# Kernel tuning notes

Measured on AMD Instinct MI355X. Metric: run time of the kernel, lower is better.

Reference implementation:

```python
import jax, jax.numpy as jnp
import numpy as np

B = 2048
D = 40960          # util.half_kp_numel(): 64 king squares * 640 piece-square planes
BASE = 288
MOVE = 4096        # util.move_numel(): 64 from-squares * 64 to-squares
MOVE_SIZE = (64, 64)


def setup_inputs() -> dict:
    key = jax.random.key(0)
    ks = jax.random.split(key, 24)
    f32 = jnp.float32
    # forward args: sparse one-hot half-kp occupancy vectors (modeled as rand floats)
    pov = (jax.random.uniform(ks[0], (B, 1), f32) > 0.5).astype(f32)
    white = (jax.random.uniform(ks[1], (B, D), f32) < 0.001).astype(f32)
    black = (jax.random.uniform(ks[2], (B, D), f32) < 0.001).astype(f32)
    s = 0.01
    p = {
        'W_w': jax.random.normal(ks[3], (BASE, D), f32) * s,
        'b_w': jnp.zeros((BASE,), f32),
        'W_b': jax.random.normal(ks[4], (BASE, D), f32) * s,
        'b_b': jnp.zeros((BASE,), f32),
        'W_v0': jax.random.normal(ks[5], (32, 2 * BASE), f32) * s,
        'b_v0': jnp.zeros((32,), f32),
        'W_v1': jax.random.normal(ks[6], (32, 32), f32) * s,
        'b_v1': jnp.zeros((32,), f32),
        'W_v2': jax.random.normal(ks[7], (1, 32), f32) * s,
        'b_v2': jnp.zeros((1,), f32),
        'W_a0': jax.random.normal(ks[8], (144, 2 * BASE), f32) * s,
        'b_a0': jnp.zeros((144,), f32),
        'W_a1': jax.random.normal(ks[9], (MOVE, 144), f32) * s,
        'b_a1': jnp.zeros((MOVE,), f32),
        'W_vs': jax.random.normal(ks[10], (1, 2 * BASE), f32) * s,
        'b_vs': jnp.zeros((1,), f32),
        'W_as': jax.random.normal(ks[11], (MOVE, 2 * BASE), f32) * s,
        'b_as': jnp.zeros((MOVE,), f32),
    }
    return dict(pov=pov, white=white, black=black, **p)


def _linear(x, W, b):
    return x @ W.T + b


def reference(pov, white, black, W_w, b_w, W_b, b_b,
              W_v0, b_v0, W_v1, b_v1, W_v2, b_v2,
              W_a0, b_a0, W_a1, b_a1, W_vs, b_vs, W_as, b_as):
    # half-kp affine accumulators (the sparse gather-sum candidate)
    w256 = _linear(white, W_w, b_w)            # [B, BASE]
    b256 = _linear(black, W_b, b_b)            # [B, BASE]
    cat_wb = jnp.concatenate([w256, b256], axis=1)
    cat_bw = jnp.concatenate([b256, w256], axis=1)
    base = jax.nn.relu(pov * cat_wb + (1.0 - pov) * cat_bw)  # [B, 2*BASE]
    # value head with skip
    val = jax.nn.relu(_linear(base, W_v0, b_v0))
    val = jax.nn.relu(_linear(val, W_v1, b_v1))
    val = _linear(val, W_v2, b_v2) + _linear(base, W_vs, b_vs)   # [B, 1]
    # action head with skip
    act = jax.nn.relu(_linear(base, W_a0, b_a0))
    act = _linear(act, W_a1, b_a1) + _linear(base, W_as, b_as)   # [B, MOVE]
    act = act.reshape(act.shape[0], *MOVE_SIZE)                  # [B, 64, 64]
    return (val, act)
```

## Files before the change

### kernel.cpp

```cpp
#include <hip/hip_runtime.h>

#define D_IN 40960
#define NB 2048
#define BASEN 288
#define CAPL 95
#define KP 736

typedef __attribute__((ext_vector_type(4))) float f32x4;
typedef __attribute__((ext_vector_type(8))) short short8;

__device__ inline float bf2f(ushort u) {
    unsigned v = ((unsigned)u) << 16; float f; __builtin_memcpy(&f, &v, 4); return f;
}
__device__ inline ushort f2bf(float f) {
    unsigned x; __builtin_memcpy(&x, &f, 4);
    unsigned r = (x + 0x7FFFu + ((x >> 16) & 1u)) >> 16; return (ushort)r;
}

__device__ inline void llds16(const void* g, void* l) {
    __builtin_amdgcn_global_load_lds((const __attribute__((address_space(1))) unsigned*)g,
                                     (__attribute__((address_space(3))) unsigned*)l, 16, 0, 0);
}

__global__ __launch_bounds__(256) void transpose_kernel(const float* __restrict__ Ww,
                                                        const float* __restrict__ Wb,
                                                        ushort* __restrict__ Wtw,
                                                        ushort* __restrict__ Wtb) {
    const float* src = blockIdx.z ? Wb : Ww;
    ushort* dst = blockIdx.z ? Wtb : Wtw;
    __shared__ float tile[32][65];
    int i = threadIdx.x;
    int d0 = blockIdx.x * 64, o0 = blockIdx.y * 32;
    int tr = i >> 4, tc4 = (i & 15) * 4;
#pragma unroll
    for (int rep = 0; rep < 2; ++rep) {
        int row = tr + rep * 16;
        float4 u = *(const float4*)&src[(size_t)(o0 + row) * D_IN + d0 + tc4];
        tile[row][tc4] = u.x; tile[row][tc4 + 1] = u.y; tile[row][tc4 + 2] = u.z; tile[row][tc4 + 3] = u.w;
    }
    __syncthreads();
    int dr = i >> 3, oc4 = (i & 7) * 4;
#pragma unroll
    for (int rep = 0; rep < 2; ++rep) {
        int d = dr + rep * 32;
        ushort4 u;
        u.x = f2bf(tile[oc4][d]); u.y = f2bf(tile[oc4 + 1][d]);
        u.z = f2bf(tile[oc4 + 2][d]); u.w = f2bf(tile[oc4 + 3][d]);
        *(ushort4*)&dst[(size_t)(d0 + d) * BASEN + o0 + oc4] = u;
    }
}

__global__ __launch_bounds__(256) void prep_kernel(const float* __restrict__ W_a1,
                                                   const float* __restrict__ W_as,
                                                   const float* __restrict__ b_a1,
                                                   const float* __restrict__ b_as,
                                                   const float* __restrict__ W_a0,
                                                   const float* __restrict__ W_v0,
                                                   ushort* __restrict__ Wcat,
                                                   float* __restrict__ biasA,
                                                   ushort* __restrict__ Wa0h,
                                                   ushort* __restrict__ Wv0h) {
    int m = blockIdx.x, t = threadIdx.x;
    if (m < 4096) {
        ushort* dst = Wcat + (size_t)m * KP;
        if (t < 144) dst[t] = f2bf(W_a1[(size_t)m * 144 + t]);
        if (t >= 144 && t < 160) dst[t] = 0;
        for (int j = t; j < 576; j += 256) dst[160 + j] = f2bf(W_as[(size_t)m * 576 + j]);
        if (t == 200) biasA[m] = b_a1[m] + b_as[m];
    } else if (m < 4096 + 144) {
        int r = m - 4096;
        for (int j = t; j < 576; j += 256) Wa0h[(size_t)r * 576 + j] = f2bf(W_a0[(size_t)r * 576 + j]);
    } else {
        int r = m - (4096 + 144);
        for (int j = t; j < 576; j += 256) Wv0h[(size_t)r * 576 + j] = f2bf(W_v0[(size_t)r * 576 + j]);
    }
}

__global__ __launch_bounds__(576) void row_kernel(const float* __restrict__ white,
                                                  const float* __restrict__ black,
                                                  const ushort* __restrict__ Wtw,
                                                  const ushort* __restrict__ Wtb,
                                                  const float* __restrict__ pov,
                                                  const float* __restrict__ b_w,
                                                  const float* __restrict__ b_b,
                                                  const ushort* __restrict__ Wa0h,
                                                  const float* __restrict__ b_a0,
                                                  const ushort* __restrict__ Wv0h,
                                                  const float* __restrict__ b_v0,
                                                  const float* __restrict__ W_v1,
                                                  const float* __restrict__ b_v1,
                                                  const float* __restrict__ W_v2,
                                                  const float* __restrict__ b_v2,
                                                  const float* __restrict__ W_vs,
                                                  const float* __restrict__ b_vs,
                                                  ushort* __restrict__ hidden,
                                                  float* __restrict__ outv) {
    int b = blockIdx.x, t = threadIdx.x;
    __shared__ int cntW, cntB;
    __shared__ int idxW[CAPL], idxB[CAPL];
    __shared__ float accS[576];
    __shared__ float baseS[576];
    __shared__ float v0s[32];
    __shared__ float skipS;
    if (t == 0) cntW = 0;
    if (t == 1) cntB = 0;
    __syncthreads();

    const uint4* vw = (const uint4*)(white + (size_t)b * D_IN);
    const uint4* vb = (const uint4*)(black + (size_t)b * D_IN);
    for (int i = t; i < D_IN / 4; i += 576) {
        uint4 x = vw[i];
        if (x.x) { int p = atomicAdd(&cntW, 1); if (p < CAPL) idxW[p] = i * 4; }
        if (x.y) { int p = atomicAdd(&cntW, 1); if (p < CAPL) idxW[p] = i * 4 + 1; }
        if (x.z) { int p = atomicAdd(&cntW, 1); if (p < CAPL) idxW[p] = i * 4 + 2; }
        if (x.w) { int p = atomicAdd(&cntW, 1); if (p < CAPL) idxW[p] = i * 4 + 3; }
        uint4 y = vb[i];
        if (y.x) { int p = atomicAdd(&cntB, 1); if (p < CAPL) idxB[p] = i * 4; }
        if (y.y) { int p = atomicAdd(&cntB, 1); if (p < CAPL) idxB[p] = i * 4 + 1; }
        if (y.z) { int p = atomicAdd(&cntB, 1); if (p < CAPL) idxB[p] = i * 4 + 2; }
        if (y.w) { int p = atomicAdd(&cntB, 1); if (p < CAPL) idxB[p] = i * 4 + 3; }
    }
    __syncthreads();

    {
        int col = (t < 288) ? t : t - 288;
        const ushort* Wt = (t < 288) ? Wtw : Wtb;
        const int* il = (t < 288) ? idxW : idxB;
        int n = min((t < 288) ? cntW : cntB, CAPL);
        float acc = (t < 288) ? b_w[col] : b_b[col];
#pragma unroll 4
        for (int i = 0; i < n; ++i) acc += bf2f(Wt[(size_t)il[i] * BASEN + col]);
        accS[t] = acc;
    }
    __syncthreads();

    float p = pov[b];
    ushort* hrow = hidden + (size_t)b * KP;
    if (t < 288) {
        float aW = accS[t], aB = accS[288 + t];
        float b0 = fmaxf(p * aW + (1.0f - p) * aB, 0.0f);
        float b1 = fmaxf(p * aB + (1.0f - p) * aW, 0.0f);
        baseS[t] = b0; baseS[288 + t] = b1;
        hrow[160 + t] = f2bf(b0);
        hrow[160 + 288 + t] = f2bf(b1);
        if (t < 16) hrow[144 + t] = 0;
    }
    __syncthreads();

    {
        int o = t >> 2, q4 = t & 3;
        const ushort* wr = Wa0h + (size_t)o * 576 + q4 * 144;
        const float* bp = &baseS[q4 * 144];
        float s = 0.f;
#pragma unroll
        for (int j = 0; j < 144; j += 8) {
            uint4 q = *(const uint4*)(wr + j);
            s += bp[j + 0] * bf2f((ushort)(q.x & 0xFFFF)) + bp[j + 1] * bf2f((ushort)(q.x >> 16))
               + bp[j + 2] * bf2f((ushort)(q.y & 0xFFFF)) + bp[j + 3] * bf2f((ushort)(q.y >> 16))
               + bp[j + 4] * bf2f((ushort)(q.z & 0xFFFF)) + bp[j + 5] * bf2f((ushort)(q.z >> 16))
               + bp[j + 6] * bf2f((ushort)(q.w & 0xFFFF)) + bp[j + 7] * bf2f((ushort)(q.w >> 16));
        }
        s += __shfl_xor(s, 1);
        s += __shfl_xor(s, 2);
        if (q4 == 0) hrow[o] = f2bf(fmaxf(s + b_a0[o], 0.f));
    }

    if (t < 512) {
        int o = t >> 4, sub = t & 15;
        const ushort* wr = Wv0h + (size_t)o * 576 + sub * 36;
        const float* bp = &baseS[sub * 36];
        float s = 0.f;
#pragma unroll
        for (int j = 0; j < 36; j += 4) {
            ushort4 q = *(const ushort4*)(wr + j);
            s += bp[j + 0] * bf2f(q.x) + bp[j + 1] * bf2f(q.y)
               + bp[j + 2] * bf2f(q.z) + bp[j + 3] * bf2f(q.w);
        }
        s += __shfl_xor(s, 1); s += __shfl_xor(s, 2);
        s += __shfl_xor(s, 4); s += __shfl_xor(s, 8);
        if (sub == 0) v0s[o] = fmaxf(s + b_v0[o], 0.f);
    } else {
        int u = t - 512;
        const float* wp = W_vs + u * 9;
        const float* bp = &baseS[u * 9];
        float s = 0.f;
#pragma unroll
        for (int j = 0; j < 9; ++j) s += bp[j] * wp[j];
        s += __shfl_xor(s, 1); s += __shfl_xor(s, 2); s += __shfl_xor(s, 4);
        s += __shfl_xor(s, 8); s += __shfl_xor(s, 16); s += __shfl_xor(s, 32);
        if (u == 0) skipS = s;
    }
    __syncthreads();

    if (t < 32) {
        float s = b_v1[t];
        const float* w = W_v1 + (size_t)t * 32;
#pragma unroll
        for (int j = 0; j < 32; ++j) s += v0s[j] * w[j];
        float part = fmaxf(s, 0.f) * W_v2[t];
        part += __shfl_xor(part, 1); part += __shfl_xor(part, 2); part += __shfl_xor(part, 4);
        part += __shfl_xor(part, 8); part += __shfl_xor(part, 16);
        if (t == 0) outv[b] = part + b_v2[0] + skipS + b_vs[0];
    }
}

__global__ __launch_bounds__(256) void gemm_act(const ushort* __restrict__ A,
                                                const ushort* __restrict__ Bm,
                                                const float* __restrict__ biasA,
                                                float* __restrict__ outa) {
    __shared__ ushort As[128 * 32];
    __shared__ ushort Bs[128 * 32];
    int tid = threadIdx.x;
    int lane = tid & 63, wv = tid >> 6;
    int bm = blockIdx.x, bn = blockIdx.y;
    int wm = wv & 1, wn = wv >> 1;
    f32x4 acc[4][4];
#pragma unroll
    for (int mt = 0; mt < 4; ++mt)
#pragma unroll
        for (int nt = 0; nt < 4; ++nt) { f32x4 z = {0.f, 0.f, 0.f, 0.f}; acc[mt][nt] = z; }

    int r = tid >> 2, c8 = (tid & 3) * 8;
    const ushort* Ag = A  + (size_t)(bm * 128 + r) * KP + c8;
    const ushort* Bg = Bm + (size_t)(bn * 128 + r) * KP + c8;
    ushort* AsW = As + wv * 512;
    ushort* BsW = Bs + wv * 512;

    int kg = (lane >> 4) * 8;
    int rA = wm * 64 + (lane & 15);
    int rB = wn * 64 + (lane & 15);

    for (int kk = 0; kk < KP; kk += 32) {
        llds16(Ag + kk, AsW);
        llds16(Ag + (size_t)64 * KP + kk, AsW + 2048);
        llds16(Bg + kk, BsW);
        llds16(Bg + (size_t)64 * KP + kk, BsW + 2048);
        __syncthreads();
        short8 af[4], bf[4];
#pragma unroll
        for (int mt = 0; mt < 4; ++mt) af[mt] = *(const short8*)&As[(rA + mt * 16) * 32 + kg];
#pragma unroll
        for (int nt = 0; nt < 4; ++nt) bf[nt] = *(const short8*)&Bs[(rB + nt * 16) * 32 + kg];
#pragma unroll
        for (int mt = 0; mt < 4; ++mt)
#pragma unroll
            for (int nt = 0; nt < 4; ++nt)
                acc[mt][nt] = __builtin_amdgcn_mfma_f32_16x16x32_bf16(af[mt], bf[nt], acc[mt][nt], 0, 0, 0);
        __syncthreads();
    }

    int colb = bn * 128 + wn * 64 + (lane & 15);
    int rowb = bm * 128 + wm * 64 + ((lane >> 4) << 2);
#pragma unroll
    for (int nt = 0; nt < 4; ++nt) {
        float bia = biasA[colb + nt * 16];
#pragma unroll
        for (int mt = 0; mt < 4; ++mt) {
#pragma unroll
            for (int q = 0; q < 4; ++q) {
                int rr = rowb + mt * 16 + q;
                outa[(size_t)rr * 4096 + colb + nt * 16] = acc[mt][nt][q] + bia;
            }
        }
    }
}

extern "C" void kernel_launch(void* const* d_in, const int* in_sizes, int n_in,
                              void* d_out, int out_size, void* d_ws, size_t ws_size,
                              hipStream_t stream) {
    const float* pov   = (const float*)d_in[0];
    const float* white = (const float*)d_in[1];
    const float* black = (const float*)d_in[2];
    const float* W_w   = (const float*)d_in[3];
    const float* b_w   = (const float*)d_in[4];
    const float* W_b   = (const float*)d_in[5];
    const float* b_b   = (const float*)d_in[6];
    const float* W_v0  = (const float*)d_in[7];
    const float* b_v0  = (const float*)d_in[8];
    const float* W_v1  = (const float*)d_in[9];
    const float* b_v1  = (const float*)d_in[10];
    const float* W_v2  = (const float*)d_in[11];
    const float* b_v2  = (const float*)d_in[12];
    const float* W_a0  = (const float*)d_in[13];
    const float* b_a0  = (const float*)d_in[14];
    const float* W_a1  = (const float*)d_in[15];
    const float* b_a1  = (const float*)d_in[16];
    const float* W_vs  = (const float*)d_in[17];
    const float* b_vs  = (const float*)d_in[18];
    const float* W_as  = (const float*)d_in[19];
    const float* b_as  = (const float*)d_in[20];

    char* ws = (char*)d_ws;
    ushort* Wtw   = (ushort*)(ws + 0);
    ushort* Wtb   = (ushort*)(ws + 23592960);
    ushort* hidden= (ushort*)(ws + 47185920);
    ushort* Wcat  = (ushort*)(ws + 50200576);
    float*  biasA = (float*)(ws + 56229888);
    ushort* Wa0h  = (ushort*)(ws + 56246272);
    ushort* Wv0h  = (ushort*)(ws + 56412160);

    float* outp = (float*)d_out;

    transpose_kernel<<<dim3(D_IN / 64, BASEN / 32, 2), 256, 0, stream>>>(W_w, W_b, Wtw, Wtb);
    prep_kernel<<<4096 + 144 + 32, 256, 0, stream>>>(W_a1, W_as, b_a1, b_as, W_a0, W_v0,
                                                     Wcat, biasA, Wa0h, Wv0h);
    row_kernel<<<NB, 576, 0, stream>>>(white, black, Wtw, Wtb, pov, b_w, b_b,
                                       Wa0h, b_a0, Wv0h, b_v0, W_v1, b_v1, W_v2, b_v2,
                                       W_vs, b_vs, hidden, outp);
    gemm_act<<<dim3(2048 / 128, 4096 / 128), 256, 0, stream>>>(hidden, Wcat, biasA, outp + 2048);
}
```

Before: 871.8 us.

## Split sparse index scan into separate wide-grid kernel with global atomics

```diff
diff --git a/kernel.cpp b/kernel.cpp
--- a/kernel.cpp
+++ b/kernel.cpp
@@ -4,7 +4,10 @@
 #define NB 2048
 #define BASEN 288
 #define CAPL 95
+#define LSTRIDE 96
 #define KP 736
+#define SPLITS 4
+#define CHUNK (D_IN / 4 / SPLITS)
 
 typedef __attribute__((ext_vector_type(4))) float f32x4;
 typedef __attribute__((ext_vector_type(8))) short short8;
@@ -20,6 +23,36 @@
 __device__ inline void llds16(const void* g, void* l) {
     __builtin_amdgcn_global_load_lds((const __attribute__((address_space(1))) unsigned*)g,
                                      (__attribute__((address_space(3))) unsigned*)l, 16, 0, 0);
+}
+
+__global__ __launch_bounds__(256) void zcnt_kernel(int* __restrict__ lists) {
+    int t = blockIdx.x * 256 + threadIdx.x;
+    if (t < 2 * NB) lists[(size_t)t * LSTRIDE] = 0;
+}
+
+__global__ __launch_bounds__(256) void scan_kernel(const float* __restrict__ white,
+                                                   const float* __restrict__ black,
+                                                   int* __restrict__ lists) {
+    int b = blockIdx.x, c = blockIdx.y, s = blockIdx.z;
+    int t = threadIdx.x;
+    const uint4* v = (const uint4*)((c ? black : white) + (size_t)b * D_IN) + s * CHUNK;
+    int* dst = lists + ((size_t)c * NB + b) * LSTRIDE;
+    int base4 = s * CHUNK * 4;
+
+    uint4 x = v[t];
+#pragma unroll
+    for (int k = 0; k < CHUNK / 256; ++k) {
+        uint4 xn;
+        if (k < CHUNK / 256 - 1) xn = v[t + (k + 1) * 256];
+        if (x.x | x.y | x.z | x.w) {
+            int i4 = base4 + (t + k * 256) * 4;
+            if (x.x) { int p = atomicAdd(dst, 1); if (p < CAPL) dst[1 + p] = i4; }
+            if (x.y) { int p = atomicAdd(dst, 1); if (p < CAPL) dst[1 + p] = i4 + 1; }
+            if (x.z) { int p = atomicAdd(dst, 1); if (p < CAPL) dst[1 + p] = i4 + 2; }
+            if (x.w) { int p = atomicAdd(dst, 1); if (p < CAPL) dst[1 + p] = i4 + 3; }
+        }
+        x = xn;
+    }
 }
 
 __global__ __launch_bounds__(256) void transpose_kernel(const float* __restrict__ Ww,
@@ -76,8 +109,7 @@
     }
 }
 
-__global__ __launch_bounds__(576) void row_kernel(const float* __restrict__ white,
-                                                  const float* __restrict__ black,
+__global__ __launch_bounds__(576) void row_kernel(const int* __restrict__ lists,
                                                   const ushort* __restrict__ Wtw,
                                                   const ushort* __restrict__ Wtb,
                                                   const float* __restrict__ pov,
@@ -96,37 +128,23 @@
                                                   ushort* __restrict__ hidden,
                                                   float* __restrict__ outv) {
     int b = blockIdx.x, t = threadIdx.x;
-    __shared__ int cntW, cntB;
+    __shared__ int cnts[2];
     __shared__ int idxW[CAPL], idxB[CAPL];
     __shared__ float accS[576];
     __shared__ float baseS[576];
     __shared__ float v0s[32];
     __shared__ float skipS;
-    if (t == 0) cntW = 0;
-    if (t == 1) cntB = 0;
-    __syncthreads();
-
-    const uint4* vw = (const uint4*)(white + (size_t)b * D_IN);
-    const uint4* vb = (const uint4*)(black + (size_t)b * D_IN);
-    for (int i = t; i < D_IN / 4; i += 576) {
-        uint4 x = vw[i];
-        if (x.x) { int p = atomicAdd(&cntW, 1); if (p < CAPL) idxW[p] = i * 4; }
-        if (x.y) { int p = atomicAdd(&cntW, 1); if (p < CAPL) idxW[p] = i * 4 + 1; }
-        if (x.z) { int p = atomicAdd(&cntW, 1); if (p < CAPL) idxW[p] = i * 4 + 2; }
-        if (x.w) { int p = atomicAdd(&cntW, 1); if (p < CAPL) idxW[p] = i * 4 + 3; }
-        uint4 y = vb[i];
-        if (y.x) { int p = atomicAdd(&cntB, 1); if (p < CAPL) idxB[p] = i * 4; }
-        if (y.y) { int p = atomicAdd(&cntB, 1); if (p < CAPL) idxB[p] = i * 4 + 1; }
-        if (y.z) { int p = atomicAdd(&cntB, 1); if (p < CAPL) idxB[p] = i * 4 + 2; }
-        if (y.w) { int p = atomicAdd(&cntB, 1); if (p < CAPL) idxB[p] = i * 4 + 3; }
-    }
+    const int* lw = lists + (size_t)b * LSTRIDE;
+    const int* lb = lists + ((size_t)NB + b) * LSTRIDE;
+    if (t < 2) cnts[t] = min((t == 0 ? lw[0] : lb[0]), CAPL);
+    for (int i = t; i < CAPL; i += 576) { idxW[i] = lw[1 + i]; idxB[i] = lb[1 + i]; }
     __syncthreads();
 
     {
         int col = (t < 288) ? t : t - 288;
         const ushort* Wt = (t < 288) ? Wtw : Wtb;
         const int* il = (t < 288) ? idxW : idxB;
-        int n = min((t < 288) ? cntW : cntB, CAPL);
+        int n = cnts[t < 288 ? 0 : 1];
         float acc = (t < 288) ? b_w[col] : b_b[col];
 #pragma unroll 4
         for (int i = 0; i < n; ++i) acc += bf2f(Wt[(size_t)il[i] * BASEN + col]);
@@ -298,13 +316,16 @@
     float*  biasA = (float*)(ws + 56229888);
     ushort* Wa0h  = (ushort*)(ws + 56246272);
     ushort* Wv0h  = (ushort*)(ws + 56412160);
+    int*    lists = (int*)  (ws + 56449024);
 
     float* outp = (float*)d_out;
 
+    zcnt_kernel<<<16, 256, 0, stream>>>(lists);
+    scan_kernel<<<dim3(NB, 2, SPLITS), 256, 0, stream>>>(white, black, lists);
     transpose_kernel<<<dim3(D_IN / 64, BASEN / 32, 2), 256, 0, stream>>>(W_w, W_b, Wtw, Wtb);
     prep_kernel<<<4096 + 144 + 32, 256, 0, stream>>>(W_a1, W_as, b_a1, b_as, W_a0, W_v0,
                                                      Wcat, biasA, Wa0h, Wv0h);
-    row_kernel<<<NB, 576, 0, stream>>>(white, black, Wtw, Wtb, pov, b_w, b_b,
+    row_kernel<<<NB, 576, 0, stream>>>(lists, Wtw, Wtb, pov, b_w, b_b,
                                        Wa0h, b_a0, Wv0h, b_v0, W_v1, b_v1, W_v2, b_v2,
                                        W_vs, b_vs, hidden, outp);
     gemm_act<<<dim3(2048 / 128, 4096 / 128), 256, 0, stream>>>(hidden, Wcat, biasA, outp + 2048);
```

New measurement: 880.3 us. No clear change (+1.0%).
